# Performance work log

Measured on AMD Instinct MI355X. Metric: run time of the kernel, lower is better.

## Reference

```python
import jax, jax.numpy as jnp
import numpy as np

N_UPDATE = 3

def _lin(key, fan_in, fan_out):
    s = 1.0 / np.sqrt(fan_in)
    k1, k2 = jax.random.split(key)
    W = jax.random.uniform(k1, (fan_in, fan_out), jnp.float32, -s, s)
    b = jax.random.uniform(k2, (fan_out,), jnp.float32, -s, s)
    return W, b

def setup_inputs() -> dict:
    key = jax.random.key(0)
    ks = jax.random.split(key, 12)
    N, E, F_NODE, F_EDGE, H, L, R, T = 50000, 400000, 16, 16, 32, 64, 128, 1
    inp = {}
    inp["x"] = jax.random.normal(ks[0], (N, F_NODE), jnp.float32)
    inp["edge_index"] = jax.random.randint(ks[1], (E, 2), 0, N)  # [E,2] (src,dst)
    inp["edge_attr"] = jax.random.normal(ks[2], (E, F_EDGE), jnp.float32)
    # edge MLP: F_EDGE -> 64 -> 64 -> H*H
    inp["Wm0"], inp["bm0"] = _lin(ks[3], F_EDGE, L)
    inp["Wm1"], inp["bm1"] = _lin(ks[4], L, L)
    inp["Wm2"], inp["bm2"] = _lin(ks[5], L, H * H)
    # NNConv root weight + bias
    inp["root"], inp["bias"] = _lin(ks[6], H, H)
    # readout i-net: 2H -> R -> T ; j-net: H -> R -> T
    inp["Wi0"], inp["bi0"] = _lin(ks[7], 2 * H, R)
    inp["Wi1"], inp["bi1"] = _lin(ks[8], R, T)
    inp["Wj0"], inp["bj0"] = _lin(ks[9], H, R)
    inp["Wj1"], inp["bj1"] = _lin(ks[10], R, T)
    return inp

def reference(x, edge_index, edge_attr, Wm0, bm0, Wm1, bm1, Wm2, bm2,
              root, bias, Wi0, bi0, Wi1, bi1, Wj0, bj0, Wj1, bj1):
    N = x.shape[0]
    H = root.shape[0]
    # h_0 = [x, zeros] padded to hidden_state_size
    h0 = jnp.concatenate([x, jnp.zeros((N, H - x.shape[1]), x.dtype)], axis=1)
    # edge MLP -> per-edge weight matrices (edge_attr constant across updates)
    e = jax.nn.relu(edge_attr @ Wm0 + bm0)
    e = jax.nn.relu(e @ Wm1 + bm1)
    W = (e @ Wm2 + bm2).reshape(-1, H, H)  # [E, H, H]
    src = edge_index[:, 0]
    dst = edge_index[:, 1]
    h = h0
    for _ in range(N_UPDATE):
        msg = jnp.einsum('eh,eho->eo', h[src], W)              # gather + bmm
        agg = jax.ops.segment_sum(msg, dst, num_segments=N)    # scatter-add
        h = h @ root + bias + agg                              # NNConv root/bias
    # mpnn readout: sum_v sigmoid(i([h_T, h_0])) * j(h_T)
    gate = jax.nn.sigmoid(jax.nn.relu(jnp.concatenate([h, h0], 1) @ Wi0 + bi0) @ Wi1 + bi1)
    val = jax.nn.relu(h @ Wj0 + bj0) @ Wj1 + bj1
    return jnp.sum(gate * val, axis=0)  # [target_size]
```

## Files before the change

### kernel.cpp

```cpp
#include <hip/hip_runtime.h>
#include <stdint.h>

#define N_UPDATE 3
#define HD 32
#define FN 16

typedef unsigned short u16;
typedef __bf16 bf16x8 __attribute__((ext_vector_type(8)));
typedef float f32x4 __attribute__((ext_vector_type(4)));

__device__ __forceinline__ float bf2f(u16 u) {
  union { uint32_t i; float f; } v; v.i = ((uint32_t)u) << 16; return v.f;
}
__device__ __forceinline__ u16 f2bf(float f) {
  union { uint32_t i; float f; } v; v.f = f;
  uint32_t x = v.i;
  return (u16)((x + 0x7fffu + ((x >> 16) & 1u)) >> 16);
}

union frag16 { uint4 v; bf16x8 b; u16 s[8]; };

__global__ void k_zero_i(int* __restrict__ p, int n) {
  int i = blockIdx.x * blockDim.x + threadIdx.x;
  if (i < n) p[i] = 0;
}

__global__ void k_hist2(const int* __restrict__ eidx, int* __restrict__ cntS,
                        int* __restrict__ cntD, int E) {
  int e = blockIdx.x * blockDim.x + threadIdx.x;
  if (e >= E) return;
  int2 sd = ((const int2*)eidx)[e];
  atomicAdd(&cntS[sd.x], 1);
  atomicAdd(&cntD[sd.y], 1);
}

__global__ __launch_bounds__(1024) void k_scan(const int* __restrict__ cnt,
                                               int* __restrict__ out1,
                                               int* __restrict__ out2, int N) {
  __shared__ int sums[1024];
  int chunk = (N + 1023) / 1024;
  int beg = threadIdx.x * chunk;
  int end = beg + chunk; if (end > N) end = N;
  if (beg > N) beg = N;
  int s = 0;
  for (int i = beg; i < end; i++) s += cnt[i];
  sums[threadIdx.x] = s;
  __syncthreads();
  for (int off = 1; off < 1024; off <<= 1) {
    int v = (threadIdx.x >= off) ? sums[threadIdx.x - off] : 0;
    __syncthreads();
    sums[threadIdx.x] += v;
    __syncthreads();
  }
  int run = (threadIdx.x == 0) ? 0 : sums[threadIdx.x - 1];
  for (int i = beg; i < end; i++) {
    out1[i] = run;
    if (out2) out2[i] = run;
    run += cnt[i];
  }
  if (end == N) {
    out1[N] = run;
    if (out2) out2[N] = run;
  }
}

__global__ void k_scatter(const int* __restrict__ eidx, int* __restrict__ ptrS,
                          int* __restrict__ ptrD, int2* __restrict__ spd,
                          int* __restrict__ invp, int E) {
  int e = blockIdx.x * blockDim.x + threadIdx.x;
  if (e >= E) return;
  int2 sd = ((const int2*)eidx)[e];
  int pos = atomicAdd(&ptrS[sd.x], 1);
  int dpos = atomicAdd(&ptrD[sd.y], 1);
  spd[pos] = make_int2(sd.x, dpos);
  invp[e] = pos;
}

__global__ void k_prep_bf(const float* __restrict__ Wm2, uint4* __restrict__ Bf) {
  int t = blockIdx.x;
  int lane = threadIdx.x;
  int col = lane & 15;
  int hg = lane >> 4;
  int p = t >> 6;
  int t2 = t & 63;
  int j2 = t2 * 16 + col;
  int o = p * 16 + (j2 >> 6);
  int k = j2 & 63;
  frag16 f;
#pragma unroll
  for (int jj = 0; jj < 8; jj++) {
    int h = hg * 8 + jj;
    f.s[jj] = f2bf(Wm2[k * 1024 + h * 32 + o]);
  }
  Bf[t * 64 + lane] = f.v;
}

__global__ void k_init_h(const float* __restrict__ x, const float* __restrict__ bm2,
                         float* __restrict__ h, float* __restrict__ hbbuf, int N) {
  int idx = blockIdx.x * blockDim.x + threadIdx.x;
  if (idx >= N * HD) return;
  int n = idx >> 5, o = idx & 31;
  float v = (o < FN) ? x[n * FN + o] : 0.f;
  h[idx] = v;
  float hb = 0.f;
#pragma unroll
  for (int k = 0; k < 32; k++)
    hb = fmaf(__shfl(v, k, 32), bm2[k * 32 + o], hb);
  hbbuf[idx] = hb;
}

__global__ __launch_bounds__(256, 2) void k_edge_mlp(
    const float* __restrict__ ea,
    const float* __restrict__ Wm0, const float* __restrict__ bm0,
    const float* __restrict__ Wm1, const float* __restrict__ bm1,
    const int* __restrict__ invp, u16* __restrict__ ee, int E) {
  int e = blockIdx.x * blockDim.x + threadIdx.x;
  if (e >= E) return;
  float a[16];
  {
    const float4* p = (const float4*)(ea + (size_t)e * 16);
    float4 v0 = p[0], v1 = p[1], v2 = p[2], v3 = p[3];
    a[0]=v0.x; a[1]=v0.y; a[2]=v0.z; a[3]=v0.w;
    a[4]=v1.x; a[5]=v1.y; a[6]=v1.z; a[7]=v1.w;
    a[8]=v2.x; a[9]=v2.y; a[10]=v2.z; a[11]=v2.w;
    a[12]=v3.x; a[13]=v3.y; a[14]=v3.z; a[15]=v3.w;
  }
  float t0[64];
#pragma unroll
  for (int j = 0; j < 64; j++) t0[j] = bm0[j];
#pragma unroll
  for (int k = 0; k < 16; k++) {
    float av = a[k];
#pragma unroll
    for (int j = 0; j < 64; j++) t0[j] = fmaf(av, Wm0[k * 64 + j], t0[j]);
  }
#pragma unroll
  for (int j = 0; j < 64; j++) t0[j] = fmaxf(t0[j], 0.f);

  u16* dst = ee + (size_t)invp[e] * 64;
#pragma unroll
  for (int half = 0; half < 2; half++) {
    float t1[32];
#pragma unroll
    for (int j = 0; j < 32; j++) t1[j] = bm1[half * 32 + j];
#pragma unroll
    for (int k = 0; k < 64; k++) {
      float tv = t0[k];
#pragma unroll
      for (int j = 0; j < 32; j++) t1[j] = fmaf(tv, Wm1[k * 64 + half * 32 + j], t1[j]);
    }
    unsigned int out[16];
#pragma unroll
    for (int j = 0; j < 16; j++) {
      u16 lo = f2bf(fmaxf(t1[2 * j], 0.f));
      u16 hi = f2bf(fmaxf(t1[2 * j + 1], 0.f));
      out[j] = (unsigned int)lo | ((unsigned int)hi << 16);
    }
    uint4* op = (uint4*)(dst + half * 32);
#pragma unroll
    for (int q = 0; q < 4; q++) {
      uint4 w; w.x = out[q*4+0]; w.y = out[q*4+1]; w.z = out[q*4+2]; w.w = out[q*4+3];
      op[q] = w;
    }
  }
}

__global__ __launch_bounds__(256) void k_gemm_G(
    const float* __restrict__ h, const uint4* __restrict__ Bf,
    u16* __restrict__ Gb, int N, int p) {
  int wave = threadIdx.x >> 6;
  int lane = threadIdx.x & 63;
  int jt = blockIdx.y * 4 + wave;
  int n0 = blockIdx.x * 16;
  int row = lane & 15;
  int kg = lane >> 4;

  int nr = n0 + row; if (nr > N - 1) nr = N - 1;
  const float* hr = h + (size_t)nr * HD + kg * 8;
  float4 f0 = *(const float4*)hr;
  float4 f1 = *(const float4*)(hr + 4);
  frag16 a;
  a.s[0] = f2bf(f0.x); a.s[1] = f2bf(f0.y); a.s[2] = f2bf(f0.z); a.s[3] = f2bf(f0.w);
  a.s[4] = f2bf(f1.x); a.s[5] = f2bf(f1.y); a.s[6] = f2bf(f1.z); a.s[7] = f2bf(f1.w);

  frag16 b; b.v = Bf[(p * 64 + jt) * 64 + lane];

  f32x4 acc = {0.f, 0.f, 0.f, 0.f};
  acc = __builtin_amdgcn_mfma_f32_16x16x32_bf16(a.b, b.b, acc, 0, 0, 0);

  int o_l = jt >> 2;
  int k = (jt & 3) * 16 + row;
  int idx = (k >> 3) * 128 + o_l * 8 + (k & 7);
#pragma unroll
  for (int r = 0; r < 4; r++) {
    int n = n0 + kg * 4 + r;
    if (n < N) Gb[(size_t)n * 1024 + idx] = f2bf(acc[r]);
  }
}

__global__ __launch_bounds__(256) void k_msg(
    const u16* __restrict__ Gb, const float* __restrict__ hbbuf,
    const u16* __restrict__ ee, const int2* __restrict__ spd,
    float* __restrict__ msgbuf, int E, int p) {
  int t = blockIdx.x * blockDim.x + threadIdx.x;
  int e = t >> 4;
  int o_l = t & 15;
  if (e >= E) return;
  int2 sp = spd[e];

  float acc = hbbuf[(size_t)sp.x * HD + p * 16 + o_l];

  const uint4* ep = (const uint4*)(ee + (size_t)e * 64);
  const uint4* gp = (const uint4*)(Gb + (size_t)sp.x * 1024);
  frag16 eu[8], gu[8];
#pragma unroll
  for (int q = 0; q < 8; q++) {
    eu[q].v = ep[q];
    gu[q].v = gp[q * 16 + o_l];
  }
#pragma unroll
  for (int k = 0; k < 64; k++) {
    acc = fmaf(bf2f(eu[k >> 3].s[k & 7]), bf2f(gu[k >> 3].s[k & 7]), acc);
  }
  msgbuf[(size_t)sp.y * HD + p * 16 + o_l] = acc;
}

__global__ __launch_bounds__(256) void k_aggupd(
    const float* __restrict__ msgbuf, const int* __restrict__ rowptrD,
    const float* __restrict__ h, const float* __restrict__ root,
    const float* __restrict__ bias, const float* __restrict__ bm2,
    float* __restrict__ hn, float* __restrict__ hbbuf, int N) {
  int t = blockIdx.x * blockDim.x + threadIdx.x;
  int n = t >> 5, o = t & 31;
  if (n >= N) return;
  int jb = rowptrD[n], je = rowptrD[n + 1];
  float s = 0.f;
  for (int j = jb; j < je; j++) s += msgbuf[(size_t)j * HD + o];

  float hv = h[(size_t)n * HD + o];
  float acc = bias[o] + s;
#pragma unroll
  for (int k = 0; k < 32; k++)
    acc = fmaf(__shfl(hv, k, 32), root[k * HD + o], acc);
  hn[(size_t)n * HD + o] = acc;

  float hb = 0.f;
#pragma unroll
  for (int k = 0; k < 32; k++)
    hb = fmaf(__shfl(acc, k, 32), bm2[k * 32 + o], hb);
  hbbuf[(size_t)n * HD + o] = hb;
}

__global__ __launch_bounds__(256) void k_readout(
    const float* __restrict__ h, const float* __restrict__ x,
    const float* __restrict__ Wi0, const float* __restrict__ bi0,
    const float* __restrict__ Wi1, const float* __restrict__ bi1,
    const float* __restrict__ Wj0, const float* __restrict__ bj0,
    const float* __restrict__ Wj1, const float* __restrict__ bj1,
    float* __restrict__ partial, int N) {
  int wid = threadIdx.x >> 6;
  int lane = threadIdx.x & 63;
  int n = blockIdx.x * 4 + wid;
  __shared__ float sred[4];
  float contrib = 0.f;
  if (n < N) {
    float uv;
    if (lane < 32) uv = h[(size_t)n * HD + lane];
    else if (lane < 48) uv = x[(size_t)n * FN + lane - 32];
    else uv = 0.f;

    float g1a = bi0[lane], g1b = bi0[lane + 64];
#pragma unroll
    for (int k = 0; k < 64; k++) {
      float u = __shfl(uv, k, 64);
      g1a = fmaf(u, Wi0[k * 128 + lane], g1a);
      g1b = fmaf(u, Wi0[k * 128 + lane + 64], g1b);
    }
    g1a = fmaxf(g1a, 0.f); g1b = fmaxf(g1b, 0.f);
    float gp = g1a * Wi1[lane] + g1b * Wi1[lane + 64];

    float v1a = bj0[lane], v1b = bj0[lane + 64];
#pragma unroll
    for (int k = 0; k < 32; k++) {
      float hk = __shfl(uv, k, 64);
      v1a = fmaf(hk, Wj0[k * 128 + lane], v1a);
      v1b = fmaf(hk, Wj0[k * 128 + lane + 64], v1b);
    }
    v1a = fmaxf(v1a, 0.f); v1b = fmaxf(v1b, 0.f);
    float vp = v1a * Wj1[lane] + v1b * Wj1[lane + 64];

#pragma unroll
    for (int s = 32; s; s >>= 1) {
      gp += __shfl_xor(gp, s, 64);
      vp += __shfl_xor(vp, s, 64);
    }
    float gate = 1.f / (1.f + __expf(-(gp + bi1[0])));
    float val = vp + bj1[0];
    contrib = gate * val;
  }
  if (lane == 0) sred[wid] = contrib;
  __syncthreads();
  if (threadIdx.x == 0) partial[blockIdx.x] = sred[0] + sred[1] + sred[2] + sred[3];
}

__global__ void k_final(const float* __restrict__ partial, float* __restrict__ out, int P) {
  __shared__ float sm[256];
  float s = 0.f;
  for (int i = threadIdx.x; i < P; i += 256) s += partial[i];
  sm[threadIdx.x] = s;
  __syncthreads();
  for (int st = 128; st; st >>= 1) {
    if ((int)threadIdx.x < st) sm[threadIdx.x] += sm[threadIdx.x + st];
    __syncthreads();
  }
  if (threadIdx.x == 0) out[0] = sm[0];
}

extern "C" void kernel_launch(void* const* d_in, const int* in_sizes, int n_in,
                              void* d_out, int out_size, void* d_ws, size_t ws_size,
                              hipStream_t stream) {
  const float* x    = (const float*)d_in[0];
  const int*   eidx = (const int*)d_in[1];
  const float* ea   = (const float*)d_in[2];
  const float* Wm0  = (const float*)d_in[3];
  const float* bm0  = (const float*)d_in[4];
  const float* Wm1  = (const float*)d_in[5];
  const float* bm1  = (const float*)d_in[6];
  const float* Wm2  = (const float*)d_in[7];
  const float* bm2  = (const float*)d_in[8];
  const float* root = (const float*)d_in[9];
  const float* bias = (const float*)d_in[10];
  const float* Wi0  = (const float*)d_in[11];
  const float* bi0  = (const float*)d_in[12];
  const float* Wi1  = (const float*)d_in[13];
  const float* bi1  = (const float*)d_in[14];
  const float* Wj0  = (const float*)d_in[15];
  const float* bj0  = (const float*)d_in[16];
  const float* Wj1  = (const float*)d_in[17];
  const float* bj1  = (const float*)d_in[18];

  int N = in_sizes[0] / FN;
  int E = in_sizes[1] / 2;
  int nb = (N + 3) / 4;

  auto al = [](size_t b) { return (b + 255) & ~(size_t)255; };
  size_t need = al((size_t)N * 1024 * 2)
              + al((size_t)E * 64 * 2)
              + al((size_t)E * HD * 4)
              + al(128 * 64 * sizeof(uint4))
              + 3 * al((size_t)N * HD * 4)
              + 2 * al((size_t)N * 4)
              + 3 * al(((size_t)N + 1) * 4)
              + al((size_t)E * 8)
              + al((size_t)E * 4)
              + al((size_t)nb * 4);
  if (need > ws_size) return;

  char* ws = (char*)d_ws;
  size_t off = 0;
  auto alloc = [&](size_t bytes) { void* p = ws + off; off += al(bytes); return p; };
  u16*   Gb      = (u16*)alloc((size_t)N * 1024 * 2);
  u16*   ee      = (u16*)alloc((size_t)E * 64 * 2);
  float* msgbuf  = (float*)alloc((size_t)E * HD * 4);
  uint4* Bf      = (uint4*)alloc(128 * 64 * sizeof(uint4));
  float* hA      = (float*)alloc((size_t)N * HD * 4);
  float* hB      = (float*)alloc((size_t)N * HD * 4);
  float* hbbuf   = (float*)alloc((size_t)N * HD * 4);
  int*   cntS    = (int*)alloc((size_t)N * 4);
  int*   cntD    = (int*)alloc((size_t)N * 4);
  int*   ptrS    = (int*)alloc(((size_t)N + 1) * 4);
  int*   rowptrD = (int*)alloc(((size_t)N + 1) * 4);
  int*   ptrD    = (int*)alloc(((size_t)N + 1) * 4);
  int2*  spd     = (int2*)alloc((size_t)E * 8);
  int*   invp    = (int*)alloc((size_t)E * 4);
  float* partial = (float*)alloc((size_t)nb * 4);

  int mt = (N + 15) / 16;
  int ng = (N * HD + 255) / 256;
  int eg = (E + 255) / 256;

  int zn = (int)(((char*)cntD - (char*)cntS) / 4) + N;
  hipLaunchKernelGGL(k_zero_i, dim3((zn + 255) / 256), dim3(256), 0, stream, cntS, zn);
  hipLaunchKernelGGL(k_hist2, dim3(eg), dim3(256), 0, stream, eidx, cntS, cntD, E);
  hipLaunchKernelGGL(k_scan, dim3(1), dim3(1024), 0, stream, cntS, ptrS, (int*)nullptr, N);
  hipLaunchKernelGGL(k_scan, dim3(1), dim3(1024), 0, stream, cntD, rowptrD, ptrD, N);
  hipLaunchKernelGGL(k_scatter, dim3(eg), dim3(256), 0, stream,
                     eidx, ptrS, ptrD, spd, invp, E);

  hipLaunchKernelGGL(k_prep_bf, dim3(128), dim3(64), 0, stream, Wm2, Bf);
  hipLaunchKernelGGL(k_init_h, dim3(ng), dim3(256), 0, stream, x, bm2, hA, hbbuf, N);
  hipLaunchKernelGGL(k_edge_mlp, dim3(eg), dim3(256), 0, stream,
                     ea, Wm0, bm0, Wm1, bm1, invp, ee, E);

  float* hc = hA; float* hn = hB;
  for (int it = 0; it < N_UPDATE; it++) {
    for (int p = 0; p < 2; p++) {
      hipLaunchKernelGGL(k_gemm_G, dim3(mt, 16), dim3(256), 0, stream, hc, Bf, Gb, N, p);
      hipLaunchKernelGGL(k_msg, dim3(((size_t)E * 16 + 255) / 256), dim3(256), 0, stream,
                         Gb, hbbuf, ee, spd, msgbuf, E, p);
    }
    hipLaunchKernelGGL(k_aggupd, dim3(ng), dim3(256), 0, stream,
                       msgbuf, rowptrD, hc, root, bias, bm2, hn, hbbuf, N);
    float* tmp = hc; hc = hn; hn = tmp;
  }

  hipLaunchKernelGGL(k_readout, dim3(nb), dim3(256), 0, stream,
                     hc, x, Wi0, bi0, Wi1, bi1, Wj0, bj0, Wj1, bj1, partial, N);
  hipLaunchKernelGGL(k_final, dim3(1), dim3(256), 0, stream, partial, (float*)d_out, nb);
}
```

Before: 1.651 ms.

## Restructure message kernel to one wavefront per source node reusing G fragments

The message kernel now assigns a 64-lane wavefront to each source node and loops over that node's outgoing edges, which are contiguous in source-sorted order. The node's G row and hbbuf slice are loaded once into registers and reused for every edge instead of being re-gathered per edge. This needs a source row-pointer array, so the scan kernel now also writes rowptrS. The trade-off is load imbalance and idle lanes on nodes with few or no edges, since degrees vary. The edge MLP kernel's launch-bounds occupancy hint is also dropped.

```diff
diff --git a/kernel.cpp b/kernel.cpp
--- a/kernel.cpp
+++ b/kernel.cpp
@@ -109,7 +109,7 @@
   hbbuf[idx] = hb;
 }
 
-__global__ __launch_bounds__(256, 2) void k_edge_mlp(
+__global__ __launch_bounds__(256) void k_edge_mlp(
     const float* __restrict__ ea,
     const float* __restrict__ Wm0, const float* __restrict__ bm0,
     const float* __restrict__ Wm1, const float* __restrict__ bm1,
@@ -200,29 +200,34 @@
 
 __global__ __launch_bounds__(256) void k_msg(
     const u16* __restrict__ Gb, const float* __restrict__ hbbuf,
-    const u16* __restrict__ ee, const int2* __restrict__ spd,
-    float* __restrict__ msgbuf, int E, int p) {
-  int t = blockIdx.x * blockDim.x + threadIdx.x;
-  int e = t >> 4;
-  int o_l = t & 15;
-  if (e >= E) return;
-  int2 sp = spd[e];
-
-  float acc = hbbuf[(size_t)sp.x * HD + p * 16 + o_l];
-
-  const uint4* ep = (const uint4*)(ee + (size_t)e * 64);
-  const uint4* gp = (const uint4*)(Gb + (size_t)sp.x * 1024);
-  frag16 eu[8], gu[8];
-#pragma unroll
-  for (int q = 0; q < 8; q++) {
-    eu[q].v = ep[q];
-    gu[q].v = gp[q * 16 + o_l];
-  }
-#pragma unroll
-  for (int k = 0; k < 64; k++) {
-    acc = fmaf(bf2f(eu[k >> 3].s[k & 7]), bf2f(gu[k >> 3].s[k & 7]), acc);
-  }
-  msgbuf[(size_t)sp.y * HD + p * 16 + o_l] = acc;
+    const u16* __restrict__ ee, const int* __restrict__ rowptrS,
+    const int2* __restrict__ spd, float* __restrict__ msgbuf, int N, int p) {
+  int w = blockIdx.x * 4 + (threadIdx.x >> 6);
+  if (w >= N) return;
+  int l = threadIdx.x & 63;
+  int o_l = l & 15;
+  int g = l >> 4;
+  int jb = rowptrS[w], je = rowptrS[w + 1];
+  if (jb >= je) return;
+
+  float hbv = hbbuf[(size_t)w * HD + p * 16 + o_l];
+  const uint4* gp = (const uint4*)(Gb + (size_t)w * 1024);
+  frag16 gu[8];
+#pragma unroll
+  for (int q = 0; q < 8; q++) gu[q].v = gp[q * 16 + o_l];
+
+  for (int j0 = jb + g; j0 < je; j0 += 4) {
+    const uint4* ep = (const uint4*)(ee + (size_t)j0 * 64);
+    frag16 eu[8];
+#pragma unroll
+    for (int q = 0; q < 8; q++) eu[q].v = ep[q];
+    float acc = hbv;
+#pragma unroll
+    for (int k = 0; k < 64; k++)
+      acc = fmaf(bf2f(eu[k >> 3].s[k & 7]), bf2f(gu[k >> 3].s[k & 7]), acc);
+    int dp = spd[j0].y;
+    msgbuf[(size_t)dp * HD + p * 16 + o_l] = acc;
+  }
 }
 
 __global__ __launch_bounds__(256) void k_aggupd(
@@ -350,7 +355,7 @@
               + al(128 * 64 * sizeof(uint4))
               + 3 * al((size_t)N * HD * 4)
               + 2 * al((size_t)N * 4)
-              + 3 * al(((size_t)N + 1) * 4)
+              + 4 * al(((size_t)N + 1) * 4)
               + al((size_t)E * 8)
               + al((size_t)E * 4)
               + al((size_t)nb * 4);
@@ -369,6 +374,7 @@
   int*   cntS    = (int*)alloc((size_t)N * 4);
   int*   cntD    = (int*)alloc((size_t)N * 4);
   int*   ptrS    = (int*)alloc(((size_t)N + 1) * 4);
+  int*   rowptrS = (int*)alloc(((size_t)N + 1) * 4);
   int*   rowptrD = (int*)alloc(((size_t)N + 1) * 4);
   int*   ptrD    = (int*)alloc(((size_t)N + 1) * 4);
   int2*  spd     = (int2*)alloc((size_t)E * 8);
@@ -382,7 +388,7 @@
   int zn = (int)(((char*)cntD - (char*)cntS) / 4) + N;
   hipLaunchKernelGGL(k_zero_i, dim3((zn + 255) / 256), dim3(256), 0, stream, cntS, zn);
   hipLaunchKernelGGL(k_hist2, dim3(eg), dim3(256), 0, stream, eidx, cntS, cntD, E);
-  hipLaunchKernelGGL(k_scan, dim3(1), dim3(1024), 0, stream, cntS, ptrS, (int*)nullptr, N);
+  hipLaunchKernelGGL(k_scan, dim3(1), dim3(1024), 0, stream, cntS, ptrS, rowptrS, N);
   hipLaunchKernelGGL(k_scan, dim3(1), dim3(1024), 0, stream, cntD, rowptrD, ptrD, N);
   hipLaunchKernelGGL(k_scatter, dim3(eg), dim3(256), 0, stream,
                      eidx, ptrS, ptrD, spd, invp, E);
@@ -396,8 +402,8 @@
   for (int it = 0; it < N_UPDATE; it++) {
     for (int p = 0; p < 2; p++) {
       hipLaunchKernelGGL(k_gemm_G, dim3(mt, 16), dim3(256), 0, stream, hc, Bf, Gb, N, p);
-      hipLaunchKernelGGL(k_msg, dim3(((size_t)E * 16 + 255) / 256), dim3(256), 0, stream,
-                         Gb, hbbuf, ee, spd, msgbuf, E, p);
+      hipLaunchKernelGGL(k_msg, dim3((N + 3) / 4), dim3(256), 0, stream,
+                         Gb, hbbuf, ee, rowptrS, spd, msgbuf, N, p);
     }
     hipLaunchKernelGGL(k_aggupd, dim3(ng), dim3(256), 0, stream,
                        msgbuf, rowptrD, hc, root, bias, bm2, hn, hbbuf, N);
```

Result: slower. 1.891 ms (+14.5%).
